# Kernel optimization log

Hardware: AMD Instinct MI355X
Metric: run time of the kernel (lower is better)

The kernel has to match this reference:

```python
import jax, jax.numpy as jnp
import numpy as np

DIM = 768
NUM_HEADS = 12
N_DIV = 8
T_SHIFT = 20
T_SPAN = 11
T_CUT = T_SHIFT + 1 - T_SPAN  # 10
C = DIM // NUM_HEADS          # 64 channels per head
FOLD = C // N_DIV             # 8
BATCH = 2
FRAMES = 32
K_WIN = 4
N_TOK = 196
B_TOT = BATCH * FRAMES * K_WIN  # 256


def _entmax15_last(x):
    """Exact entmax-1.5 (Peters & Martins) along the last axis."""
    x = (x - jnp.max(x, axis=-1, keepdims=True)) * 0.5
    xs = jnp.flip(jnp.sort(x, axis=-1), axis=-1)  # descending
    d = x.shape[-1]
    rho = jnp.arange(1, d + 1, dtype=x.dtype)
    mean = jnp.cumsum(xs, axis=-1) / rho
    meansq = jnp.cumsum(xs * xs, axis=-1) / rho
    ss = rho * (meansq - mean * mean)
    delta = (1.0 - ss) / rho
    pos = delta > 0
    sq = jnp.where(pos, jnp.sqrt(jnp.where(pos, delta, 1.0)), 0.0)
    tau = mean - sq
    support = jnp.sum(tau <= xs, axis=-1, keepdims=True)
    tau_star = jnp.take_along_axis(tau, support - 1, axis=-1)
    y = jnp.clip(x - tau_star, 0.0, None)
    return y * y


def entmax15(x, axis):
    return jnp.moveaxis(_entmax15_last(jnp.moveaxis(x, axis, -1)), -1, axis)


def _shift(feat, pool_w, pool_b, win_w, win_b, forward):
    # feat: [b, t, k, h, n, c]
    b, t, k, h, n, c = feat.shape
    f = N_DIV
    cp = c // f
    # 'b t k h n (c f) -> (k n h c) (b f) t'
    g = feat.reshape(b, t, k, h, n, cp, f)
    g = jnp.transpose(g, (2, 4, 3, 5, 0, 6, 1)).reshape(k * n * h * cp, b * f, t)
    pad = (T_SHIFT, 0) if forward else (0, T_SHIFT)
    g = jnp.pad(g, ((0, 0), (0, 0), pad))
    # 'b t k h n c -> b (k n t) (h c)'
    xk = jnp.transpose(feat, (0, 2, 4, 1, 3, 5)).reshape(b, k * n * t, h * c)
    attn = xk @ pool_w + pool_b                      # [b, knt, 1]
    pooled = jnp.sum(entmax15(attn, axis=1) * xk, axis=1)  # [b, dim]
    # 'b 1 (T f) -> (b f) 1 T'
    win = (pooled @ win_w + win_b).reshape(b, T_SPAN, f)
    win = jnp.transpose(win, (0, 2, 1)).reshape(b * f, 1, T_SPAN)
    win = _entmax15_last(win)
    # depthwise conv over the (b f) channel dim, batch dim = k*n*h*cp
    out = jax.lax.conv_general_dilated(
        g, win, (1,), 'VALID',
        dimension_numbers=('NCH', 'OIH', 'NCH'),
        feature_group_count=b * f)
    tp = t + T_CUT
    # '(k n h c) (b f) t -> b t k h n c f' then mean over f
    out = out.reshape(k, n, h, cp, b, f, tp)
    out = jnp.transpose(out, (4, 6, 0, 2, 1, 3, 5)).mean(axis=-1)  # [b, tp, k, h, n, cp]
    return out[:, :-T_CUT] if forward else out[:, T_CUT:]


def _pcs(x, batch_size, frame_len, fpw, fpb, bpw, bpb, fww, fwb, bww, bwb):
    B, h, n, c = x.shape
    k = B // (batch_size * frame_len)
    feat = x.reshape(batch_size, frame_len, k, h, n, c)
    fwd = _shift(feat, fpw, fpb, fww, fwb, True)
    bwd = _shift(feat, bpw, bpb, bww, bwb, False)
    out = jnp.concatenate([fwd, bwd, feat[..., 2 * FOLD:]], axis=-1)
    return out.reshape(B, h, n, c)


def setup_inputs() -> dict:
    key = jax.random.key(0)
    ks = jax.random.split(key, 6)
    s = 0.02
    return {
        'x': jax.random.normal(ks[0], (B_TOT, NUM_HEADS, N_TOK, C), dtype=jnp.float32),
        'batch_size': BATCH,
        'frame_len': FRAMES,
        'fwd_pool_w': jax.random.normal(ks[1], (DIM, 1), dtype=jnp.float32) * s,
        'fwd_pool_b': jnp.zeros((1,), dtype=jnp.float32),
        'bwd_pool_w': jax.random.normal(ks[2], (DIM, 1), dtype=jnp.float32) * s,
        'bwd_pool_b': jnp.zeros((1,), dtype=jnp.float32),
        'fwd_win_w': jax.random.normal(ks[3], (DIM, T_SPAN * N_DIV), dtype=jnp.float32) * s,
        'fwd_win_b': jnp.zeros((T_SPAN * N_DIV,), dtype=jnp.float32),
        'bwd_win_w': jax.random.normal(ks[4], (DIM, T_SPAN * N_DIV), dtype=jnp.float32) * s,
        'bwd_win_b': jnp.zeros((T_SPAN * N_DIV,), dtype=jnp.float32),
    }


def reference(x, batch_size, frame_len, fwd_pool_w, fwd_pool_b, bwd_pool_w, bwd_pool_b,
              fwd_win_w, fwd_win_b, bwd_win_w, bwd_win_b):
    return _pcs(x, batch_size, frame_len, fwd_pool_w, fwd_pool_b, bwd_pool_w, bwd_pool_b,
                fwd_win_w, fwd_win_b, bwd_win_w, bwd_win_b)
```

## Files before the change

kernel.cpp:

```cpp
#include <hip/hip_runtime.h>

#define NH 12
#define NTOK 196
#define TT 32
#define KW 4
#define NI 25088
#define TSTRIDE 602112
#define NBLK 512
#define NWAVES (NBLK * 4)

__device__ int g_counter1;
__device__ int g_flag1;
__device__ int g_counter2;
__device__ int g_flag2;

__global__ __launch_bounds__(256, 2) void k_fused(
    const float* __restrict__ x, const float4* __restrict__ wf4,
    const float4* __restrict__ wb4,
    const float* __restrict__ fww, const float* __restrict__ fwb,
    const float* __restrict__ bww, const float* __restrict__ bwb,
    float* __restrict__ attn, float* __restrict__ winb,
    float* __restrict__ out)
{
  __shared__ float4 swf[192], swb[192];
  __shared__ int   sidx[4096];
  __shared__ float swgt[4096];
  __shared__ float spool4[4][768];
  __shared__ float spool[768];
  __shared__ float part[2][88];
  __shared__ float praw[88];
  __shared__ float sred1[4], sred2[4];
  __shared__ float sbc;
  __shared__ int   scnt, sticket, ssetter;

  int tid = threadIdx.x;
  int wave = tid >> 6, lane = tid & 63;
  if (tid < 192) { swf[tid] = wf4[tid]; swb[tid] = wb4[tid]; }
  __syncthreads();

  const float4* x4 = (const float4*)x;
  int gw = blockIdx.x * 4 + wave;
  int c4 = lane & 15, nq = lane >> 4;
  for (int tsk = gw; tsk < 256 * 49; tsk += NWAVES) {
    int B = tsk / 49, ngrp = tsk % 49;
    int n = ngrp * 4 + nq;
    float accf = 0.f, accb = 0.f;
    #pragma unroll
    for (int h = 0; h < NH; h++) {
      float4 xv = x4[((B * NH + h) * NTOK + n) * 16 + c4];
      float4 wf = swf[h * 16 + c4], wb = swb[h * 16 + c4];
      accf += xv.x * wf.x + xv.y * wf.y + xv.z * wf.z + xv.w * wf.w;
      accb += xv.x * wb.x + xv.y * wb.y + xv.z * wb.z + xv.w * wb.w;
    }
    #pragma unroll
    for (int m = 1; m < 16; m <<= 1) {
      accf += __shfl_xor(accf, m);
      accb += __shfl_xor(accb, m);
    }
    if ((lane & 15) == 0) {
      int b = B >> 7, t = (B >> 2) & 31, k = B & 3;
      int i = (k * NTOK + n) * TT + t;
      attn[b * NI + i] = accf;
      attn[(2 + b) * NI + i] = accb;
    }
  }
  __syncthreads();
  if (tid == 0)
    sticket = __hip_atomic_fetch_add(&g_counter1, 1, __ATOMIC_ACQ_REL,
                                     __HIP_MEMORY_SCOPE_AGENT);
  __syncthreads();
  int ticket = sticket;
  int iter = ticket / NBLK, rank = ticket % NBLK;
  int target = iter + 1;

  if (rank == NBLK - 1 && tid == 0)
    __hip_atomic_store(&g_flag1, target, __ATOMIC_RELEASE,
                       __HIP_MEMORY_SCOPE_AGENT);

  bool need_spin2 = true;

  if (rank >= NBLK - 4) {
    if (rank != NBLK - 1) {
      int spins = 0;
      while (__hip_atomic_load(&g_flag1, __ATOMIC_RELAXED,
                               __HIP_MEMORY_SCOPE_AGENT) < target) {
        __builtin_amdgcn_s_sleep(2);
        if (++spins > (1 << 20)) break;
      }
      (void)__hip_atomic_load(&g_flag1, __ATOMIC_ACQUIRE,
                              __HIP_MEMORY_SCOPE_AGENT);
    }
    int p = rank - (NBLK - 4);
    int b = p & 1;
    const float* a = attn + p * NI;

    float v[98];
    float mx = -3.0e38f;
    #pragma unroll
    for (int r = 0; r < 98; r++) {
      v[r] = a[r * 256 + tid];
      mx = fmaxf(mx, v[r]);
    }
    #pragma unroll
    for (int m = 1; m < 64; m <<= 1) mx = fmaxf(mx, __shfl_xor(mx, m));
    if (lane == 0) sred1[wave] = mx;
    __syncthreads();
    if (tid == 0)
      sbc = fmaxf(fmaxf(sred1[0], sred1[1]), fmaxf(sred1[2], sred1[3]));
    __syncthreads();
    float amax = sbc;
    #pragma unroll
    for (int r = 0; r < 98; r++) v[r] = 0.5f * (v[r] - amax);

    float tau = -1.0f;
    for (int it = 0; it < 8; it++) {
      float s2 = 0.f, s1 = 0.f;
      #pragma unroll
      for (int r = 0; r < 98; r++) {
        float d = fmaxf(v[r] - tau, 0.f);
        s2 += d * d;
        s1 += d;
      }
      #pragma unroll
      for (int m = 1; m < 64; m <<= 1) {
        s2 += __shfl_xor(s2, m);
        s1 += __shfl_xor(s1, m);
      }
      if (lane == 0) { sred2[wave] = s2; sred1[wave] = s1; }
      __syncthreads();
      if (tid == 0) {
        float S2 = sred2[0] + sred2[1] + sred2[2] + sred2[3];
        float S1 = sred1[0] + sred1[1] + sred1[2] + sred1[3];
        sbc = tau + (S2 - 1.f) / fmaxf(2.f * S1, 1e-12f);
      }
      __syncthreads();
      tau = sbc;
      __syncthreads();
    }

    if (tid == 0) scnt = 0;
    __syncthreads();
    #pragma unroll
    for (int r = 0; r < 98; r++) {
      float d = v[r] - tau;
      if (d > 0.f) {
        int slot = atomicAdd(&scnt, 1);
        if (slot < 4096) { sidx[slot] = r * 256 + tid; swgt[slot] = d * d; }
      }
    }
    __syncthreads();
    int count = min(scnt, 4096);

    float acc12[12];
    #pragma unroll
    for (int h = 0; h < 12; h++) acc12[h] = 0.f;
    for (int e = wave; e < count; e += 4) {
      int i = sidx[e];
      float w = swgt[e];
      int t = i & 31, r2 = i >> 5;
      int n = r2 % NTOK, k = r2 / NTOK;
      int B = (b * TT + t) * KW + k;
      const float* xb = x + (size_t)B * (NH * NTOK * 64) + n * 64 + lane;
      #pragma unroll
      for (int h = 0; h < 12; h++) acc12[h] += w * xb[h * (NTOK * 64)];
    }
    #pragma unroll
    for (int h = 0; h < 12; h++) spool4[wave][h * 64 + lane] = acc12[h];
    __syncthreads();
    #pragma unroll
    for (int q = 0; q < 3; q++) {
      int j = q * 256 + tid;
      spool[j] = spool4[0][j] + spool4[1][j] + spool4[2][j] + spool4[3][j];
    }
    __syncthreads();

    if (tid < 176) {
      int rseg = tid / 88, col = tid % 88;
      const float* ww = (p >> 1) ? bww : fww;
      float accw = 0.f;
      #pragma unroll 8
      for (int j = 0; j < 384; j++) {
        int r = rseg * 384 + j;
        accw += spool[r] * ww[r * 88 + col];
      }
      part[rseg][col] = accw;
    }
    __syncthreads();
    if (tid < 88) {
      const float* wbv = (p >> 1) ? bwb : fwb;
      praw[tid] = wbv[tid] + part[0][tid] + part[1][tid];
    }
    __syncthreads();
    if (tid < 8) {
      int f = tid;
      float vv[11];
      float mmx = -3.0e38f;
      #pragma unroll
      for (int j = 0; j < 11; j++) { vv[j] = praw[j * 8 + f]; mmx = fmaxf(mmx, vv[j]); }
      #pragma unroll
      for (int j = 0; j < 11; j++) vv[j] = 0.5f * (vv[j] - mmx);
      float lo = -1.f, hi = 0.f;
      for (int it = 0; it < 30; it++) {
        float mid = 0.5f * (lo + hi), s = 0.f;
        #pragma unroll
        for (int j = 0; j < 11; j++) { float d = fmaxf(vv[j] - mid, 0.f); s += d * d; }
        if (s >= 1.f) lo = mid; else hi = mid;
      }
      float tw = 0.5f * (lo + hi);
      #pragma unroll
      for (int j = 0; j < 11; j++) {
        float d = fmaxf(vv[j] - tw, 0.f);
        winb[p * 88 + f * 11 + j] = d * d * 0.125f;
      }
    }
    __syncthreads();
    if (tid == 0) {
      int t2 = __hip_atomic_fetch_add(&g_counter2, 1, __ATOMIC_ACQ_REL,
                                      __HIP_MEMORY_SCOPE_AGENT);
      if ((t2 & 3) == 3) {
        __hip_atomic_store(&g_flag2, target, __ATOMIC_RELEASE,
                           __HIP_MEMORY_SCOPE_AGENT);
        ssetter = 1;
      } else ssetter = 0;
    }
    __syncthreads();
    need_spin2 = (ssetter == 0);
  } else {
    int idx = rank * 256 + tid;
    if (idx < 768 * 88 / 4) {
      float4 t1 = ((const float4*)fww)[idx];
      float4 t2 = ((const float4*)bww)[idx];
      asm volatile("" :: "v"(t1.x), "v"(t2.x));
    }
  }

  if (need_spin2) {
    int spins = 0;
    while (__hip_atomic_load(&g_flag2, __ATOMIC_RELAXED,
                             __HIP_MEMORY_SCOPE_AGENT) < target) {
      __builtin_amdgcn_s_sleep(32);
      if (++spins > (1 << 20)) break;
    }
    (void)__hip_atomic_load(&g_flag2, __ATOMIC_ACQUIRE,
                            __HIP_MEMORY_SCOPE_AGENT);
  }

  for (int tsk = gw; tsk < 96 * NTOK; tsk += NWAVES) {
    int bkh = tsk / NTOK, n = tsk % NTOK;
    int b = bkh / 48, rem = bkh % 48;
    int k = rem / 12, h = rem % 12;
    int f = lane & 7;
    float wjf[11], wjb[11];
    #pragma unroll
    for (int j = 0; j < 11; j++) {
      wjf[j] = winb[b * 88 + f * 11 + j];
      wjb[j] = winb[(2 + b) * 88 + f * 11 + j];
    }
    int base = ((b * 128 + k) * NH + h) * 12544 + n * 64 + lane;
    float xr[32];
    #pragma unroll
    for (int tp = 0; tp < 32; tp++) xr[tp] = x[base + tp * TSTRIDE];

    int src = (lane & 7) << 3;
    float val[32];
    float acc[32];

    #pragma unroll
    for (int t = 0; t < 32; t++) acc[t] = 0.f;
    #pragma unroll
    for (int tp = 0; tp <= 21; tp++) {
      #pragma unroll
      for (int j = 0; j < 11; j++) {
        int to = tp + 20 - j;
        if (to >= 0 && to < 32) acc[to] += wjf[j] * xr[tp];
      }
    }
    #pragma unroll
    for (int t = 0; t < 32; t++) {
      float s = acc[t];
      s += __shfl_xor(s, 1);
      s += __shfl_xor(s, 2);
      s += __shfl_xor(s, 4);
      float sf = __shfl(s, src);
      val[t] = (lane < 8) ? sf : xr[t];
    }

    #pragma unroll
    for (int t = 0; t < 32; t++) acc[t] = 0.f;
    #pragma unroll
    for (int tp = 10; tp < 32; tp++) {
      #pragma unroll
      for (int j = 0; j < 11; j++) {
        int to = tp - 10 - j;
        if (to >= 0 && to < 32) acc[to] += wjb[j] * xr[tp];
      }
    }
    #pragma unroll
    for (int t = 0; t < 32; t++) {
      float s = acc[t];
      s += __shfl_xor(s, 1);
      s += __shfl_xor(s, 2);
      s += __shfl_xor(s, 4);
      float sb = __shfl(s, src);
      if (lane >= 8 && lane < 16) val[t] = sb;
      __builtin_nontemporal_store(val[t], &out[base + t * TSTRIDE]);
    }
  }
}

extern "C" void kernel_launch(void* const* d_in, const int* in_sizes, int n_in,
                              void* d_out, int out_size, void* d_ws, size_t ws_size,
                              hipStream_t stream)
{
  (void)in_sizes; (void)n_in; (void)out_size; (void)ws_size;
  const float* x   = (const float*)d_in[0];
  const float* fpw = (const float*)d_in[3];
  const float* bpw = (const float*)d_in[5];
  const float* fww = (const float*)d_in[7];
  const float* fwb = (const float*)d_in[8];
  const float* bww = (const float*)d_in[9];
  const float* bwb = (const float*)d_in[10];
  float* out = (float*)d_out;

  float* W    = (float*)d_ws;
  float* attn = W;
  float* winb = attn + 4 * NI;

  k_fused<<<NBLK, 256, 0, stream>>>(x, (const float4*)fpw, (const float4*)bpw,
                                    fww, fwb, bww, bwb, attn, winb, out);
}
```

Baseline: 420.1 us.

## Split fused kernel into attention-pool kernel and separate shift-conv kernel

```diff
diff --git a/kernel.cpp b/kernel.cpp
--- a/kernel.cpp
+++ b/kernel.cpp
@@ -6,42 +6,29 @@
 #define KW 4
 #define NI 25088
 #define TSTRIDE 602112
-#define NBLK 512
-#define NWAVES (NBLK * 4)
+#define NBLKA 256
+#define NWAVESA (NBLKA * 16)
 
 __device__ int g_counter1;
 __device__ int g_flag1;
-__device__ int g_counter2;
-__device__ int g_flag2;
-
-__global__ __launch_bounds__(256, 2) void k_fused(
+
+__global__ __launch_bounds__(1024) void k_attn_pool(
     const float* __restrict__ x, const float4* __restrict__ wf4,
     const float4* __restrict__ wb4,
     const float* __restrict__ fww, const float* __restrict__ fwb,
     const float* __restrict__ bww, const float* __restrict__ bwb,
-    float* __restrict__ attn, float* __restrict__ winb,
-    float* __restrict__ out)
+    float* __restrict__ attn, float* __restrict__ winb)
 {
   __shared__ float4 swf[192], swb[192];
-  __shared__ int   sidx[4096];
-  __shared__ float swgt[4096];
-  __shared__ float spool4[4][768];
-  __shared__ float spool[768];
-  __shared__ float part[2][88];
-  __shared__ float praw[88];
-  __shared__ float sred1[4], sred2[4];
-  __shared__ float sbc;
-  __shared__ int   scnt, sticket, ssetter;
-
   int tid = threadIdx.x;
   int wave = tid >> 6, lane = tid & 63;
   if (tid < 192) { swf[tid] = wf4[tid]; swb[tid] = wb4[tid]; }
   __syncthreads();
 
   const float4* x4 = (const float4*)x;
-  int gw = blockIdx.x * 4 + wave;
+  int gw = blockIdx.x * 16 + wave;
   int c4 = lane & 15, nq = lane >> 4;
-  for (int tsk = gw; tsk < 256 * 49; tsk += NWAVES) {
+  for (int tsk = gw; tsk < 256 * 49; tsk += NWAVESA) {
     int B = tsk / 49, ngrp = tsk % 49;
     int n = ngrp * 4 + nq;
     float accf = 0.f, accb = 0.f;
@@ -65,246 +52,241 @@
     }
   }
   __syncthreads();
+
+  __shared__ int sticket;
   if (tid == 0)
     sticket = __hip_atomic_fetch_add(&g_counter1, 1, __ATOMIC_ACQ_REL,
                                      __HIP_MEMORY_SCOPE_AGENT);
   __syncthreads();
   int ticket = sticket;
-  int iter = ticket / NBLK, rank = ticket % NBLK;
-  int target = iter + 1;
-
-  if (rank == NBLK - 1 && tid == 0)
+  int rank = ticket % NBLKA;
+  int target = ticket / NBLKA + 1;
+
+  if (rank < NBLKA - 4) return;
+
+  int p = rank - (NBLKA - 4);
+  int b = p & 1;
+  const float* ww = (p >> 1) ? bww : fww;
+  const float* wbv = (p >> 1) ? bwb : fwb;
+
+  if (rank == NBLKA - 1 && tid == 0)
     __hip_atomic_store(&g_flag1, target, __ATOMIC_RELEASE,
                        __HIP_MEMORY_SCOPE_AGENT);
 
-  bool need_spin2 = true;
-
-  if (rank >= NBLK - 4) {
-    if (rank != NBLK - 1) {
-      int spins = 0;
-      while (__hip_atomic_load(&g_flag1, __ATOMIC_RELAXED,
-                               __HIP_MEMORY_SCOPE_AGENT) < target) {
-        __builtin_amdgcn_s_sleep(2);
-        if (++spins > (1 << 20)) break;
-      }
-      (void)__hip_atomic_load(&g_flag1, __ATOMIC_ACQUIRE,
-                              __HIP_MEMORY_SCOPE_AGENT);
-    }
-    int p = rank - (NBLK - 4);
-    int b = p & 1;
-    const float* a = attn + p * NI;
-
-    float v[98];
-    float mx = -3.0e38f;
-    #pragma unroll
-    for (int r = 0; r < 98; r++) {
-      v[r] = a[r * 256 + tid];
-      mx = fmaxf(mx, v[r]);
-    }
-    #pragma unroll
-    for (int m = 1; m < 64; m <<= 1) mx = fmaxf(mx, __shfl_xor(mx, m));
-    if (lane == 0) sred1[wave] = mx;
+  {
+    float dummy = 0.f;
+    const float4* ww4 = (const float4*)ww;
+    for (int q = tid; q < 768 * 88 / 4; q += 1024) {
+      float4 tv = ww4[q];
+      dummy += tv.x + tv.y + tv.z + tv.w;
+    }
+    asm volatile("" :: "v"(dummy));
+  }
+
+  if (rank != NBLKA - 1) {
+    int spins = 0;
+    while (__hip_atomic_load(&g_flag1, __ATOMIC_RELAXED,
+                             __HIP_MEMORY_SCOPE_AGENT) < target) {
+      __builtin_amdgcn_s_sleep(2);
+      if (++spins > (1 << 20)) break;
+    }
+    (void)__hip_atomic_load(&g_flag1, __ATOMIC_ACQUIRE,
+                            __HIP_MEMORY_SCOPE_AGENT);
+  }
+
+  const float* a = attn + p * NI;
+  float v[25];
+  float mx = -3.0e38f;
+  #pragma unroll
+  for (int r = 0; r < 25; r++) {
+    int i = r * 1024 + tid;
+    v[r] = (i < NI) ? a[i] : -3.0e38f;
+    mx = fmaxf(mx, v[r]);
+  }
+  __shared__ float sred1[16];
+  __shared__ float sred2[16];
+  __shared__ float sbc;
+  int wv = tid >> 6;
+  #pragma unroll
+  for (int m = 1; m < 64; m <<= 1) mx = fmaxf(mx, __shfl_xor(mx, m));
+  if ((tid & 63) == 0) sred1[wv] = mx;
+  __syncthreads();
+  if (tid == 0) {
+    float m2 = sred1[0];
+    for (int i2 = 1; i2 < 16; i2++) m2 = fmaxf(m2, sred1[i2]);
+    sbc = m2;
+  }
+  __syncthreads();
+  float amax = sbc;
+  #pragma unroll
+  for (int r = 0; r < 25; r++) v[r] = 0.5f * (v[r] - amax);
+
+  float tau = -1.0f;
+  for (int it = 0; it < 8; it++) {
+    float s2 = 0.f, s1 = 0.f;
+    #pragma unroll
+    for (int r = 0; r < 25; r++) {
+      float d = fmaxf(v[r] - tau, 0.f);
+      s2 += d * d;
+      s1 += d;
+    }
+    #pragma unroll
+    for (int m = 1; m < 64; m <<= 1) {
+      s2 += __shfl_xor(s2, m);
+      s1 += __shfl_xor(s1, m);
+    }
+    if ((tid & 63) == 0) { sred2[wv] = s2; sred1[wv] = s1; }
     __syncthreads();
-    if (tid == 0)
-      sbc = fmaxf(fmaxf(sred1[0], sred1[1]), fmaxf(sred1[2], sred1[3]));
+    if (tid == 0) {
+      float S2 = 0.f, S1 = 0.f;
+      for (int i2 = 0; i2 < 16; i2++) { S2 += sred2[i2]; S1 += sred1[i2]; }
+      sbc = tau + (S2 - 1.f) / fmaxf(2.f * S1, 1e-12f);
+    }
     __syncthreads();
-    float amax = sbc;
-    #pragma unroll
-    for (int r = 0; r < 98; r++) v[r] = 0.5f * (v[r] - amax);
-
-    float tau = -1.0f;
-    for (int it = 0; it < 8; it++) {
-      float s2 = 0.f, s1 = 0.f;
-      #pragma unroll
-      for (int r = 0; r < 98; r++) {
-        float d = fmaxf(v[r] - tau, 0.f);
-        s2 += d * d;
-        s1 += d;
-      }
-      #pragma unroll
-      for (int m = 1; m < 64; m <<= 1) {
-        s2 += __shfl_xor(s2, m);
-        s1 += __shfl_xor(s1, m);
-      }
-      if (lane == 0) { sred2[wave] = s2; sred1[wave] = s1; }
-      __syncthreads();
-      if (tid == 0) {
-        float S2 = sred2[0] + sred2[1] + sred2[2] + sred2[3];
-        float S1 = sred1[0] + sred1[1] + sred1[2] + sred1[3];
-        sbc = tau + (S2 - 1.f) / fmaxf(2.f * S1, 1e-12f);
-      }
-      __syncthreads();
-      tau = sbc;
-      __syncthreads();
-    }
-
-    if (tid == 0) scnt = 0;
+    tau = sbc;
     __syncthreads();
-    #pragma unroll
-    for (int r = 0; r < 98; r++) {
-      float d = v[r] - tau;
-      if (d > 0.f) {
-        int slot = atomicAdd(&scnt, 1);
-        if (slot < 4096) { sidx[slot] = r * 256 + tid; swgt[slot] = d * d; }
-      }
-    }
-    __syncthreads();
-    int count = min(scnt, 4096);
-
-    float acc12[12];
-    #pragma unroll
-    for (int h = 0; h < 12; h++) acc12[h] = 0.f;
-    for (int e = wave; e < count; e += 4) {
+  }
+
+  __shared__ int scnt;
+  __shared__ int sidx[8192];
+  __shared__ float swgt[8192];
+  if (tid == 0) scnt = 0;
+  __syncthreads();
+  #pragma unroll
+  for (int r = 0; r < 25; r++) {
+    float d = v[r] - tau;
+    if (d > 0.f) {
+      int slot = atomicAdd(&scnt, 1);
+      if (slot < 8192) { sidx[slot] = r * 1024 + tid; swgt[slot] = d * d; }
+    }
+  }
+  __syncthreads();
+  int count = min(scnt, 8192);
+
+  __shared__ float spool[768];
+  if (tid < 768) {
+    int h = tid >> 6, c = tid & 63;
+    float acc = 0.f;
+    for (int e = 0; e < count; e++) {
       int i = sidx[e];
       float w = swgt[e];
       int t = i & 31, r2 = i >> 5;
       int n = r2 % NTOK, k = r2 / NTOK;
       int B = (b * TT + t) * KW + k;
-      const float* xb = x + (size_t)B * (NH * NTOK * 64) + n * 64 + lane;
+      acc += w * x[((B * NH + h) * NTOK + n) * 64 + c];
+    }
+    spool[tid] = acc;
+  }
+  __syncthreads();
+
+  __shared__ float part[8][88];
+  __shared__ float praw[88];
+  if (tid < 704) {
+    int rseg = tid / 88, col = tid % 88;
+    float accw = 0.f;
+    #pragma unroll 8
+    for (int j = 0; j < 96; j++) {
+      int r = rseg * 96 + j;
+      accw += spool[r] * ww[r * 88 + col];
+    }
+    part[rseg][col] = accw;
+  }
+  __syncthreads();
+  if (tid < 88) {
+    float s = wbv[tid];
+    #pragma unroll
+    for (int g = 0; g < 8; g++) s += part[g][tid];
+    praw[tid] = s;
+  }
+  __syncthreads();
+  if (tid < 8) {
+    int f = tid;
+    float vv[11];
+    float mmx = -3.0e38f;
+    #pragma unroll
+    for (int j = 0; j < 11; j++) { vv[j] = praw[j * 8 + f]; mmx = fmaxf(mmx, vv[j]); }
+    #pragma unroll
+    for (int j = 0; j < 11; j++) vv[j] = 0.5f * (vv[j] - mmx);
+    float lo = -1.f, hi = 0.f;
+    for (int it = 0; it < 30; it++) {
+      float mid = 0.5f * (lo + hi), s = 0.f;
       #pragma unroll
-      for (int h = 0; h < 12; h++) acc12[h] += w * xb[h * (NTOK * 64)];
-    }
-    #pragma unroll
-    for (int h = 0; h < 12; h++) spool4[wave][h * 64 + lane] = acc12[h];
-    __syncthreads();
-    #pragma unroll
-    for (int q = 0; q < 3; q++) {
-      int j = q * 256 + tid;
-      spool[j] = spool4[0][j] + spool4[1][j] + spool4[2][j] + spool4[3][j];
-    }
-    __syncthreads();
-
-    if (tid < 176) {
-      int rseg = tid / 88, col = tid % 88;
-      const float* ww = (p >> 1) ? bww : fww;
-      float accw = 0.f;
-      #pragma unroll 8
-      for (int j = 0; j < 384; j++) {
-        int r = rseg * 384 + j;
-        accw += spool[r] * ww[r * 88 + col];
-      }
-      part[rseg][col] = accw;
-    }
-    __syncthreads();
-    if (tid < 88) {
-      const float* wbv = (p >> 1) ? bwb : fwb;
-      praw[tid] = wbv[tid] + part[0][tid] + part[1][tid];
-    }
-    __syncthreads();
-    if (tid < 8) {
-      int f = tid;
-      float vv[11];
-      float mmx = -3.0e38f;
-      #pragma unroll
-      for (int j = 0; j < 11; j++) { vv[j] = praw[j * 8 + f]; mmx = fmaxf(mmx, vv[j]); }
-      #pragma unroll
-      for (int j = 0; j < 11; j++) vv[j] = 0.5f * (vv[j] - mmx);
-      float lo = -1.f, hi = 0.f;
-      for (int it = 0; it < 30; it++) {
-        float mid = 0.5f * (lo + hi), s = 0.f;
-        #pragma unroll
-        for (int j = 0; j < 11; j++) { float d = fmaxf(vv[j] - mid, 0.f); s += d * d; }
-        if (s >= 1.f) lo = mid; else hi = mid;
-      }
-      float tw = 0.5f * (lo + hi);
-      #pragma unroll
-      for (int j = 0; j < 11; j++) {
-        float d = fmaxf(vv[j] - tw, 0.f);
-        winb[p * 88 + f * 11 + j] = d * d * 0.125f;
-      }
-    }
-    __syncthreads();
-    if (tid == 0) {
-      int t2 = __hip_atomic_fetch_add(&g_counter2, 1, __ATOMIC_ACQ_REL,
-                                      __HIP_MEMORY_SCOPE_AGENT);
-      if ((t2 & 3) == 3) {
-        __hip_atomic_store(&g_flag2, target, __ATOMIC_RELEASE,
-                           __HIP_MEMORY_SCOPE_AGENT);
-        ssetter = 1;
-      } else ssetter = 0;
-    }
-    __syncthreads();
-    need_spin2 = (ssetter == 0);
-  } else {
-    int idx = rank * 256 + tid;
-    if (idx < 768 * 88 / 4) {
-      float4 t1 = ((const float4*)fww)[idx];
-      float4 t2 = ((const float4*)bww)[idx];
-      asm volatile("" :: "v"(t1.x), "v"(t2.x));
-    }
-  }
-
-  if (need_spin2) {
-    int spins = 0;
-    while (__hip_atomic_load(&g_flag2, __ATOMIC_RELAXED,
-                             __HIP_MEMORY_SCOPE_AGENT) < target) {
-      __builtin_amdgcn_s_sleep(32);
-      if (++spins > (1 << 20)) break;
-    }
-    (void)__hip_atomic_load(&g_flag2, __ATOMIC_ACQUIRE,
-                            __HIP_MEMORY_SCOPE_AGENT);
-  }
-
-  for (int tsk = gw; tsk < 96 * NTOK; tsk += NWAVES) {
-    int bkh = tsk / NTOK, n = tsk % NTOK;
-    int b = bkh / 48, rem = bkh % 48;
-    int k = rem / 12, h = rem % 12;
-    int f = lane & 7;
-    float wjf[11], wjb[11];
+      for (int j = 0; j < 11; j++) { float d = fmaxf(vv[j] - mid, 0.f); s += d * d; }
+      if (s >= 1.f) lo = mid; else hi = mid;
+    }
+    float tw = 0.5f * (lo + hi);
     #pragma unroll
     for (int j = 0; j < 11; j++) {
-      wjf[j] = winb[b * 88 + f * 11 + j];
-      wjb[j] = winb[(2 + b) * 88 + f * 11 + j];
-    }
-    int base = ((b * 128 + k) * NH + h) * 12544 + n * 64 + lane;
-    float xr[32];
-    #pragma unroll
-    for (int tp = 0; tp < 32; tp++) xr[tp] = x[base + tp * TSTRIDE];
-
-    int src = (lane & 7) << 3;
-    float val[32];
-    float acc[32];
-
-    #pragma unroll
-    for (int t = 0; t < 32; t++) acc[t] = 0.f;
-    #pragma unroll
-    for (int tp = 0; tp <= 21; tp++) {
-      #pragma unroll
-      for (int j = 0; j < 11; j++) {
-        int to = tp + 20 - j;
-        if (to >= 0 && to < 32) acc[to] += wjf[j] * xr[tp];
-      }
-    }
-    #pragma unroll
-    for (int t = 0; t < 32; t++) {
-      float s = acc[t];
-      s += __shfl_xor(s, 1);
-      s += __shfl_xor(s, 2);
-      s += __shfl_xor(s, 4);
-      float sf = __shfl(s, src);
-      val[t] = (lane < 8) ? sf : xr[t];
-    }
-
-    #pragma unroll
-    for (int t = 0; t < 32; t++) acc[t] = 0.f;
-    #pragma unroll
-    for (int tp = 10; tp < 32; tp++) {
-      #pragma unroll
-      for (int j = 0; j < 11; j++) {
-        int to = tp - 10 - j;
-        if (to >= 0 && to < 32) acc[to] += wjb[j] * xr[tp];
-      }
-    }
-    #pragma unroll
-    for (int t = 0; t < 32; t++) {
-      float s = acc[t];
-      s += __shfl_xor(s, 1);
-      s += __shfl_xor(s, 2);
-      s += __shfl_xor(s, 4);
-      float sb = __shfl(s, src);
-      if (lane >= 8 && lane < 16) val[t] = sb;
-      __builtin_nontemporal_store(val[t], &out[base + t * TSTRIDE]);
-    }
+      float d = fmaxf(vv[j] - tw, 0.f);
+      winb[p * 88 + f * 11 + j] = d * d * 0.125f;
+    }
+  }
+}
+
+__global__ __launch_bounds__(256) void k_shift(
+    const float* __restrict__ x, const float* __restrict__ win,
+    float* __restrict__ out)
+{
+  int bkh = blockIdx.y;
+  int b = bkh / 48, rem = bkh % 48;
+  int k = rem / 12, h = rem % 12;
+  int wave = threadIdx.x >> 6, lane = threadIdx.x & 63;
+  int n = blockIdx.x * 4 + wave;
+  int f = lane & 7;
+  float wjf[11], wjb[11];
+  #pragma unroll
+  for (int j = 0; j < 11; j++) {
+    wjf[j] = win[b * 88 + f * 11 + j];
+    wjb[j] = win[(2 + b) * 88 + f * 11 + j];
+  }
+  int base = ((b * 128 + k) * NH + h) * 12544 + n * 64 + lane;
+  float xr[32];
+  #pragma unroll
+  for (int tp = 0; tp < 32; tp++) xr[tp] = x[base + tp * TSTRIDE];
+
+  int src = (lane & 7) << 3;
+  float val[32];
+  float acc[32];
+
+  #pragma unroll
+  for (int t = 0; t < 32; t++) acc[t] = 0.f;
+  #pragma unroll
+  for (int tp = 0; tp <= 21; tp++) {
+    #pragma unroll
+    for (int j = 0; j < 11; j++) {
+      int to = tp + 20 - j;
+      if (to >= 0 && to < 32) acc[to] += wjf[j] * xr[tp];
+    }
+  }
+  #pragma unroll
+  for (int t = 0; t < 32; t++) {
+    float s = acc[t];
+    s += __shfl_xor(s, 1);
+    s += __shfl_xor(s, 2);
+    s += __shfl_xor(s, 4);
+    float sf = __shfl(s, src);
+    val[t] = (lane < 8) ? sf : xr[t];
+  }
+
+  #pragma unroll
+  for (int t = 0; t < 32; t++) acc[t] = 0.f;
+  #pragma unroll
+  for (int tp = 10; tp < 32; tp++) {
+    #pragma unroll
+    for (int j = 0; j < 11; j++) {
+      int to = tp - 10 - j;
+      if (to >= 0 && to < 32) acc[to] += wjb[j] * xr[tp];
+    }
+  }
+  #pragma unroll
+  for (int t = 0; t < 32; t++) {
+    float s = acc[t];
+    s += __shfl_xor(s, 1);
+    s += __shfl_xor(s, 2);
+    s += __shfl_xor(s, 4);
+    float sb = __shfl(s, src);
+    if (lane >= 8 && lane < 16) val[t] = sb;
+    __builtin_nontemporal_store(val[t], &out[base + t * TSTRIDE]);
   }
 }
 
@@ -326,6 +308,9 @@
   float* attn = W;
   float* winb = attn + 4 * NI;
 
-  k_fused<<<NBLK, 256, 0, stream>>>(x, (const float4*)fpw, (const float4*)bpw,
-                                    fww, fwb, bww, bwb, attn, winb, out);
+  k_attn_pool<<<NBLKA, 1024, 0, stream>>>(x, (const float4*)fpw,
+                                          (const float4*)bpw, fww, fwb,
+                                          bww, bwb, attn, winb);
+  dim3 g5(49, 96);
+  k_shift<<<g5, 256, 0, stream>>>(x, winb, out);
 }
```

New measurement: 352.2 us. -16.2%, faster.
